# Kernel tuning notes

Measured on AMD Instinct MI355X. Metric: run time of the kernel, lower is better.

## Reference

```python
import jax, jax.numpy as jnp
import numpy as np

D_MODEL = 1024


def setup_inputs() -> dict:
    key = jax.random.key(0)
    kx, kq, kk, kv = jax.random.split(key, 4)
    x = jax.random.normal(kx, (4, 2048, D_MODEL), dtype=jnp.float32)
    s = 1.0 / np.sqrt(D_MODEL)
    # torch nn.Linear weight is [out, in]; y = x @ W.T
    Wq = jax.random.normal(kq, (D_MODEL, D_MODEL), dtype=jnp.float32) * s
    Wk = jax.random.normal(kk, (D_MODEL, D_MODEL), dtype=jnp.float32) * s
    Wv = jax.random.normal(kv, (D_MODEL, D_MODEL), dtype=jnp.float32) * s
    return {"x": x, "Wq": Wq, "Wk": Wk, "Wv": Wv}


def reference(x, Wq, Wk, Wv):
    # Linear projections (no bias): [b, s, d]
    Q = jnp.einsum("bsd,ed->bse", x, Wq)
    K = jnp.einsum("bsd,ed->bse", x, Wk)
    V = jnp.einsum("bsd,ed->bse", x, Wv)
    d_k = Q.shape[-1]
    scores = jnp.einsum("bqd,bkd->bqk", Q, K) / jnp.sqrt(jnp.asarray(d_k, Q.dtype))
    weights = jax.nn.softmax(scores, axis=-1)
    return jnp.einsum("bqk,bkd->bqd", weights, V)
```

## Files before the change

kernel.cpp:

```cpp
#include <hip/hip_runtime.h>
#include <hip/hip_bf16.h>

using bf16 = __hip_bfloat16;
typedef __attribute__((ext_vector_type(8))) short short8;
typedef __attribute__((ext_vector_type(16))) float f32x16;

__global__ __launch_bounds__(256) void cast_f32_to_bf16(const float* __restrict__ in,
                                                        bf16* __restrict__ out) {
  const int i = (blockIdx.x * 256 + threadIdx.x) * 4;
  const float4 f = *(const float4*)(in + i);
  bf16 h[4];
  h[0] = __float2bfloat16(f.x);
  h[1] = __float2bfloat16(f.y);
  h[2] = __float2bfloat16(f.z);
  h[3] = __float2bfloat16(f.w);
  *(uint2*)(out + i) = *(const uint2*)h;
}

__global__ __launch_bounds__(256) void cast_weights(const float* __restrict__ Wq,
                                                    const float* __restrict__ Wk,
                                                    const float* __restrict__ Wv,
                                                    bf16* __restrict__ out) {
  const int b = blockIdx.x;
  const float* src = (b < 1024) ? (Wq + (size_t)b * 1024)
                   : (b < 2048) ? (Wk + (size_t)(b - 1024) * 1024)
                                : (Wv + (size_t)(b - 2048) * 1024);
  const int i = threadIdx.x * 4;
  const float4 f = *(const float4*)(src + i);
  bf16 h[4];
  h[0] = __float2bfloat16(f.x);
  h[1] = __float2bfloat16(f.y);
  h[2] = __float2bfloat16(f.z);
  h[3] = __float2bfloat16(f.w);
  *(uint2*)(out + (size_t)b * 1024 + i) = *(const uint2*)h;
}

template <class Epi>
__device__ __forceinline__ void gemm128_nt(const bf16* __restrict__ A, const bf16* __restrict__ B,
                                           int lda, int ldb, int K, Epi epi) {
  __shared__ char smem[36864];
  bf16* As = (bf16*)smem;
  bf16* Bs = (bf16*)(smem + 8192);
  const int t = threadIdx.x;
  const int lane = t & 63;
  const int wave = t >> 6;
  const int wm = (wave >> 1) * 64;
  const int wn = (wave & 1) * 64;
  const int m0 = blockIdx.y * 128;
  const int n0 = blockIdx.x * 128;

  f32x16 acc[2][2];
#pragma unroll
  for (int i = 0; i < 2; ++i)
#pragma unroll
    for (int j = 0; j < 2; ++j)
#pragma unroll
      for (int r = 0; r < 16; ++r) acc[i][j][r] = 0.f;

  const int r0 = t >> 2;
  const int fsw = (r0 + (r0 >> 2)) & 3;
  const int cglob = ((t & 3) ^ fsw) << 3;
  const bf16* gA0 = A + (size_t)(m0 + r0) * lda + cglob;
  const bf16* gB0 = B + (size_t)(n0 + r0) * ldb + cglob;
  const bf16* gA1 = gA0 + (size_t)64 * lda;
  const bf16* gB1 = gB0 + (size_t)64 * ldb;
  bf16* lA = As + (size_t)wave * 64 * 8;
  bf16* lB = Bs + (size_t)wave * 64 * 8;

  const int rl = lane & 31;
  const int grp = lane >> 5;
  const int ffr = (rl + (rl >> 2)) & 3;

  for (int k0 = 0; k0 < K; k0 += 32) {
    __builtin_amdgcn_global_load_lds((const __attribute__((address_space(1))) unsigned int*)(gA0 + k0),
                                     (__attribute__((address_space(3))) unsigned int*)lA, 16, 0, 0);
    __builtin_amdgcn_global_load_lds((const __attribute__((address_space(1))) unsigned int*)(gB0 + k0),
                                     (__attribute__((address_space(3))) unsigned int*)lB, 16, 0, 0);
    __builtin_amdgcn_global_load_lds((const __attribute__((address_space(1))) unsigned int*)(gA1 + k0),
                                     (__attribute__((address_space(3))) unsigned int*)(lA + 2048), 16, 0, 0);
    __builtin_amdgcn_global_load_lds((const __attribute__((address_space(1))) unsigned int*)(gB1 + k0),
                                     (__attribute__((address_space(3))) unsigned int*)(lB + 2048), 16, 0, 0);
    __syncthreads();

    short8 af[2][2], bfr[2][2];
#pragma unroll
    for (int ks = 0; ks < 2; ++ks) {
      const int kb = ks * 2 + grp;
      const int co = ((kb ^ ffr) << 3);
#pragma unroll
      for (int mt = 0; mt < 2; ++mt)
        af[ks][mt] = *(const short8*)(As + (wm + mt * 32 + rl) * 32 + co);
#pragma unroll
      for (int nt = 0; nt < 2; ++nt)
        bfr[ks][nt] = *(const short8*)(Bs + (wn + nt * 32 + rl) * 32 + co);
    }
#pragma unroll
    for (int ks = 0; ks < 2; ++ks)
#pragma unroll
      for (int mt = 0; mt < 2; ++mt)
#pragma unroll
        for (int nt = 0; nt < 2; ++nt)
          acc[mt][nt] = __builtin_amdgcn_mfma_f32_32x32x16_bf16(af[ks][mt], bfr[ks][nt],
                                                                acc[mt][nt], 0, 0, 0);
    __syncthreads();
  }

  epi(acc, m0, n0, wm, wn, lane, wave, smem);
}

__device__ __forceinline__ int c_row(int reg, int lane) {
  return (reg & 3) + 8 * (reg >> 2) + 4 * (lane >> 5);
}

template <class F>
__device__ __forceinline__ void for_each_c(const f32x16 (&acc)[2][2], int m0, int n0, int wm,
                                           int wn, int lane, F f) {
  const int rl = lane & 31;
#pragma unroll
  for (int mt = 0; mt < 2; ++mt)
#pragma unroll
    for (int nt = 0; nt < 2; ++nt)
#pragma unroll
      for (int reg = 0; reg < 16; ++reg)
        f(m0 + wm + mt * 32 + c_row(reg, lane), n0 + wn + nt * 32 + rl, acc[mt][nt][reg]);
}

__global__ __launch_bounds__(256) void proj_kernel(const bf16* __restrict__ xb,
                                                   const bf16* __restrict__ Wb,
                                                   bf16* __restrict__ Qb, bf16* __restrict__ Kb,
                                                   bf16* __restrict__ Vt) {
  gemm128_nt(xb, Wb, 1024, 1024, 1024,
             [=](const f32x16 (&acc)[2][2], int m0, int n0, int wm, int wn, int lane, int wave,
                 char* smem) {
    if (n0 < 2048) {
      bf16* dst = (n0 < 1024) ? Qb : Kb;
      const int nb = (n0 < 1024) ? n0 : (n0 - 1024);
      for_each_c(acc, m0, nb, wm, wn, lane, [&](int m, int n, float v) {
        dst[(size_t)m * 1024 + n] = __float2bfloat16(v);
      });
    } else {
      bf16* T = (bf16*)smem + wave * 4608;
      const int rl = lane & 31;
      const int g4 = 4 * (lane >> 5);
#pragma unroll
      for (int mt = 0; mt < 2; ++mt)
#pragma unroll
        for (int nt = 0; nt < 2; ++nt)
#pragma unroll
          for (int q = 0; q < 4; ++q) {
            bf16 h4[4];
#pragma unroll
            for (int r = 0; r < 4; ++r) h4[r] = __float2bfloat16(acc[mt][nt][4 * q + r]);
            *(uint2*)(T + (nt * 32 + rl) * 72 + mt * 32 + 8 * q + g4) = *(const uint2*)h4;
          }
      asm volatile("s_waitcnt lgkmcnt(0)" ::: "memory");
      const int mbase = m0 + wm;
      const int bb = mbase >> 11;
      const int sbase = mbase & 2047;
      const int nvbase = n0 - 2048 + wn;
#pragma unroll
      for (int i = 0; i < 8; ++i) {
        const int nl = i * 8 + (lane >> 3);
        const int ml = (lane & 7) * 8;
        const short8 val = *(const short8*)(T + nl * 72 + ml);
        *(short8*)(Vt + ((size_t)bb * 1024 + nvbase + nl) * 2048 + sbase + ml) = val;
      }
    }
  });
}

__global__ __launch_bounds__(256) void qk_exp_kernel(const bf16* __restrict__ Qb,
                                                     const bf16* __restrict__ Kb,
                                                     bf16* __restrict__ E,
                                                     float* __restrict__ Lpart) {
  const int z = blockIdx.z;
  const bf16* A = Qb + (size_t)z * 2048 * 1024;
  const bf16* B = Kb + (size_t)z * 2048 * 1024;
  bf16* Ez = E + (size_t)z * 2048 * 2048;
  float* Lz = Lpart + (size_t)z * 16 * 2048;
  gemm128_nt(A, B, 1024, 1024, 1024,
             [=](const f32x16 (&acc)[2][2], int m0, int n0, int wm, int wn, int lane, int wave,
                 char* smem) {
    float* Lp = (float*)smem;
    const int rl = lane & 31;
#pragma unroll
    for (int mt = 0; mt < 2; ++mt)
#pragma unroll
      for (int reg = 0; reg < 16; ++reg) {
        const int mr = wm + mt * 32 + c_row(reg, lane);
        float s = 0.f;
#pragma unroll
        for (int nt = 0; nt < 2; ++nt) {
          const float e = __expf(acc[mt][nt][reg] * 0.03125f);
          Ez[(size_t)(m0 + mr) * 2048 + n0 + wn + nt * 32 + rl] = __float2bfloat16(e);
          s += e;
        }
        s += __shfl_xor(s, 1, 64);
        s += __shfl_xor(s, 2, 64);
        s += __shfl_xor(s, 4, 64);
        s += __shfl_xor(s, 8, 64);
        s += __shfl_xor(s, 16, 64);
        if (rl == 0) Lp[mr * 2 + (wave & 1)] = s;
      }
    __syncthreads();
    const int t = threadIdx.x;
    if (t < 128) Lz[(n0 >> 7) * 2048 + m0 + t] = Lp[t * 2 + 0] + Lp[t * 2 + 1];
  });
}

__global__ __launch_bounds__(256) void reduce_l_kernel(const float* __restrict__ Lpart,
                                                       float* __restrict__ invL) {
  const int i = blockIdx.x * 256 + threadIdx.x;
  const int z = i >> 11, m = i & 2047;
  const float* p = Lpart + (size_t)z * 16 * 2048 + m;
  float s = 0.f;
#pragma unroll
  for (int t = 0; t < 16; ++t) s += p[(size_t)t * 2048];
  invL[i] = 1.f / s;
}

__global__ __launch_bounds__(256) void pv_kernel(const bf16* __restrict__ E,
                                                 const bf16* __restrict__ Vt,
                                                 const float* __restrict__ invL,
                                                 float* __restrict__ out) {
  const int z = blockIdx.z;
  const bf16* A = E + (size_t)z * 2048 * 2048;
  const bf16* B = Vt + (size_t)z * 1024 * 2048;
  const float* ilz = invL + (size_t)z * 2048;
  float* oz = out + (size_t)z * 2048 * 1024;
  gemm128_nt(A, B, 2048, 2048, 2048,
             [=](const f32x16 (&acc)[2][2], int m0, int n0, int wm, int wn, int lane, int wave,
                 char* smem) {
    const int rl = lane & 31;
#pragma unroll
    for (int mt = 0; mt < 2; ++mt)
#pragma unroll
      for (int reg = 0; reg < 16; ++reg) {
        const int m = m0 + wm + mt * 32 + c_row(reg, lane);
        const float il = ilz[m];
#pragma unroll
        for (int nt = 0; nt < 2; ++nt)
          oz[(size_t)m * 1024 + n0 + wn + nt * 32 + rl] = acc[mt][nt][reg] * il;
      }
  });
}

extern "C" void kernel_launch(void* const* d_in, const int* in_sizes, int n_in,
                              void* d_out, int out_size, void* d_ws, size_t ws_size,
                              hipStream_t stream) {
  const float* x = (const float*)d_in[0];
  const float* Wq = (const float*)d_in[1];
  const float* Wk = (const float*)d_in[2];
  const float* Wv = (const float*)d_in[3];
  float* out = (float*)d_out;

  char* w = (char*)d_ws;
  bf16* xb = (bf16*)w; w += (size_t)8192 * 1024 * 2;
  bf16* Wb = (bf16*)w; w += (size_t)3072 * 1024 * 2;
  bf16* Qb = (bf16*)w; w += (size_t)8192 * 1024 * 2;
  bf16* Kb = (bf16*)w; w += (size_t)8192 * 1024 * 2;
  bf16* Vt = (bf16*)w; w += (size_t)8192 * 1024 * 2;
  bf16* E  = (bf16*)w; w += (size_t)4 * 2048 * 2048 * 2;
  float* Lpart = (float*)w; w += (size_t)4 * 16 * 2048 * 4;
  float* invL  = (float*)w; w += (size_t)4 * 2048 * 4;

  cast_f32_to_bf16<<<8192, 256, 0, stream>>>(x, xb);
  cast_weights<<<3072, 256, 0, stream>>>(Wq, Wk, Wv, Wb);

  proj_kernel<<<dim3(24, 64), 256, 0, stream>>>(xb, Wb, Qb, Kb, Vt);

  qk_exp_kernel<<<dim3(16, 16, 4), 256, 0, stream>>>(Qb, Kb, E, Lpart);
  reduce_l_kernel<<<32, 256, 0, stream>>>(Lpart, invL);

  pv_kernel<<<dim3(8, 16, 4), 256, 0, stream>>>(E, Vt, invL, out);
}
```

Baseline: 265.4 us.

## Double GEMM K-tile to 64, merge cast kernels, fold row-sum reduction into PV

The shared GEMM mainloop now stages a 64-wide K slice per iteration instead of 32. It uses a new 8-way XOR swizzle for global-to-LDS loads and fragment reads, which halves the number of barrier pairs per K. The two f32-to-bf16 cast kernels are merged into one launch. The separate softmax-denominator reduction kernel is removed: each PV block sums the 16 partials for its 128 rows into shared memory in its epilogue. This cuts launch overhead and synchronisation, at the cost of redundant partial-sum reads across the N blocks and a larger LDS footprint per stage.

```diff
diff --git a/kernel.cpp b/kernel.cpp
--- a/kernel.cpp
+++ b/kernel.cpp
@@ -5,26 +5,27 @@
 typedef __attribute__((ext_vector_type(8))) short short8;
 typedef __attribute__((ext_vector_type(16))) float f32x16;
 
-__global__ __launch_bounds__(256) void cast_f32_to_bf16(const float* __restrict__ in,
-                                                        bf16* __restrict__ out) {
-  const int i = (blockIdx.x * 256 + threadIdx.x) * 4;
-  const float4 f = *(const float4*)(in + i);
-  bf16 h[4];
-  h[0] = __float2bfloat16(f.x);
-  h[1] = __float2bfloat16(f.y);
-  h[2] = __float2bfloat16(f.z);
-  h[3] = __float2bfloat16(f.w);
-  *(uint2*)(out + i) = *(const uint2*)h;
-}
-
-__global__ __launch_bounds__(256) void cast_weights(const float* __restrict__ Wq,
-                                                    const float* __restrict__ Wk,
-                                                    const float* __restrict__ Wv,
-                                                    bf16* __restrict__ out) {
+__global__ __launch_bounds__(256) void cast_all(const float* __restrict__ x,
+                                                const float* __restrict__ Wq,
+                                                const float* __restrict__ Wk,
+                                                const float* __restrict__ Wv,
+                                                bf16* __restrict__ xb, bf16* __restrict__ Wb) {
   const int b = blockIdx.x;
-  const float* src = (b < 1024) ? (Wq + (size_t)b * 1024)
-                   : (b < 2048) ? (Wk + (size_t)(b - 1024) * 1024)
-                                : (Wv + (size_t)(b - 2048) * 1024);
+  const float* src;
+  bf16* dst;
+  if (b < 8192) {
+    src = x + (size_t)b * 1024;
+    dst = xb + (size_t)b * 1024;
+  } else if (b < 9216) {
+    src = Wq + (size_t)(b - 8192) * 1024;
+    dst = Wb + (size_t)(b - 8192) * 1024;
+  } else if (b < 10240) {
+    src = Wk + (size_t)(b - 9216) * 1024;
+    dst = Wb + (size_t)(b - 8192) * 1024;
+  } else {
+    src = Wv + (size_t)(b - 10240) * 1024;
+    dst = Wb + (size_t)(b - 8192) * 1024;
+  }
   const int i = threadIdx.x * 4;
   const float4 f = *(const float4*)(src + i);
   bf16 h[4];
@@ -32,7 +33,7 @@
   h[1] = __float2bfloat16(f.y);
   h[2] = __float2bfloat16(f.z);
   h[3] = __float2bfloat16(f.w);
-  *(uint2*)(out + (size_t)b * 1024 + i) = *(const uint2*)h;
+  *(uint2*)(dst + i) = *(const uint2*)h;
 }
 
 template <class Epi>
@@ -40,7 +41,7 @@
                                            int lda, int ldb, int K, Epi epi) {
   __shared__ char smem[36864];
   bf16* As = (bf16*)smem;
-  bf16* Bs = (bf16*)(smem + 8192);
+  bf16* Bs = (bf16*)(smem + 16384);
   const int t = threadIdx.x;
   const int lane = t & 63;
   const int wave = t >> 6;
@@ -57,50 +58,51 @@
 #pragma unroll
       for (int r = 0; r < 16; ++r) acc[i][j][r] = 0.f;
 
-  const int r0 = t >> 2;
-  const int fsw = (r0 + (r0 >> 2)) & 3;
-  const int cglob = ((t & 3) ^ fsw) << 3;
-  const bf16* gA0 = A + (size_t)(m0 + r0) * lda + cglob;
-  const bf16* gB0 = B + (size_t)(n0 + r0) * ldb + cglob;
-  const bf16* gA1 = gA0 + (size_t)64 * lda;
-  const bf16* gB1 = gB0 + (size_t)64 * ldb;
-  bf16* lA = As + (size_t)wave * 64 * 8;
-  bf16* lB = Bs + (size_t)wave * 64 * 8;
+  const bf16* gA[4];
+  const bf16* gB[4];
+#pragma unroll
+  for (int j = 0; j < 4; ++j) {
+    const int row = j * 32 + wave * 8 + (lane >> 3);
+    const int f = ((lane >> 3) + j * 4 + wave) & 7;
+    const int c = (((lane & 7) ^ f)) << 3;
+    gA[j] = A + (size_t)(m0 + row) * lda + c;
+    gB[j] = B + (size_t)(n0 + row) * ldb + c;
+  }
 
   const int rl = lane & 31;
   const int grp = lane >> 5;
-  const int ffr = (rl + (rl >> 2)) & 3;
-
-  for (int k0 = 0; k0 < K; k0 += 32) {
-    __builtin_amdgcn_global_load_lds((const __attribute__((address_space(1))) unsigned int*)(gA0 + k0),
-                                     (__attribute__((address_space(3))) unsigned int*)lA, 16, 0, 0);
-    __builtin_amdgcn_global_load_lds((const __attribute__((address_space(1))) unsigned int*)(gB0 + k0),
-                                     (__attribute__((address_space(3))) unsigned int*)lB, 16, 0, 0);
-    __builtin_amdgcn_global_load_lds((const __attribute__((address_space(1))) unsigned int*)(gA1 + k0),
-                                     (__attribute__((address_space(3))) unsigned int*)(lA + 2048), 16, 0, 0);
-    __builtin_amdgcn_global_load_lds((const __attribute__((address_space(1))) unsigned int*)(gB1 + k0),
-                                     (__attribute__((address_space(3))) unsigned int*)(lB + 2048), 16, 0, 0);
-    __syncthreads();
-
-    short8 af[2][2], bfr[2][2];
-#pragma unroll
-    for (int ks = 0; ks < 2; ++ks) {
+
+  for (int k0 = 0; k0 < K; k0 += 64) {
+#pragma unroll
+    for (int j = 0; j < 4; ++j) {
+      __builtin_amdgcn_global_load_lds(
+          (const __attribute__((address_space(1))) unsigned int*)(gA[j] + k0),
+          (__attribute__((address_space(3))) unsigned int*)(As + (j * 4 + wave) * 512), 16, 0, 0);
+      __builtin_amdgcn_global_load_lds(
+          (const __attribute__((address_space(1))) unsigned int*)(gB[j] + k0),
+          (__attribute__((address_space(3))) unsigned int*)(Bs + (j * 4 + wave) * 512), 16, 0, 0);
+    }
+    __syncthreads();
+
+    short8 af[4][2], bv[4][2];
+#pragma unroll
+    for (int ks = 0; ks < 4; ++ks) {
       const int kb = ks * 2 + grp;
-      const int co = ((kb ^ ffr) << 3);
+#pragma unroll
+      for (int mt = 0; mt < 2; ++mt) {
+        const int fm = (rl + (rl >> 3) + mt * 4) & 7;
+        const int co = (kb ^ fm) << 3;
+        af[ks][mt] = *(const short8*)(As + (wm + mt * 32 + rl) * 64 + co);
+        bv[ks][mt] = *(const short8*)(Bs + (wn + mt * 32 + rl) * 64 + co);
+      }
+    }
+#pragma unroll
+    for (int ks = 0; ks < 4; ++ks)
 #pragma unroll
       for (int mt = 0; mt < 2; ++mt)
-        af[ks][mt] = *(const short8*)(As + (wm + mt * 32 + rl) * 32 + co);
-#pragma unroll
-      for (int nt = 0; nt < 2; ++nt)
-        bfr[ks][nt] = *(const short8*)(Bs + (wn + nt * 32 + rl) * 32 + co);
-    }
-#pragma unroll
-    for (int ks = 0; ks < 2; ++ks)
-#pragma unroll
-      for (int mt = 0; mt < 2; ++mt)
 #pragma unroll
         for (int nt = 0; nt < 2; ++nt)
-          acc[mt][nt] = __builtin_amdgcn_mfma_f32_32x32x16_bf16(af[ks][mt], bfr[ks][nt],
+          acc[mt][nt] = __builtin_amdgcn_mfma_f32_32x32x16_bf16(af[ks][mt], bv[ks][nt],
                                                                 acc[mt][nt], 0, 0, 0);
     __syncthreads();
   }
@@ -208,39 +210,37 @@
   });
 }
 
-__global__ __launch_bounds__(256) void reduce_l_kernel(const float* __restrict__ Lpart,
-                                                       float* __restrict__ invL) {
-  const int i = blockIdx.x * 256 + threadIdx.x;
-  const int z = i >> 11, m = i & 2047;
-  const float* p = Lpart + (size_t)z * 16 * 2048 + m;
-  float s = 0.f;
-#pragma unroll
-  for (int t = 0; t < 16; ++t) s += p[(size_t)t * 2048];
-  invL[i] = 1.f / s;
-}
-
 __global__ __launch_bounds__(256) void pv_kernel(const bf16* __restrict__ E,
                                                  const bf16* __restrict__ Vt,
-                                                 const float* __restrict__ invL,
+                                                 const float* __restrict__ Lpart,
                                                  float* __restrict__ out) {
   const int z = blockIdx.z;
   const bf16* A = E + (size_t)z * 2048 * 2048;
   const bf16* B = Vt + (size_t)z * 1024 * 2048;
-  const float* ilz = invL + (size_t)z * 2048;
+  const float* Lz = Lpart + (size_t)z * 16 * 2048;
   float* oz = out + (size_t)z * 2048 * 1024;
   gemm128_nt(A, B, 2048, 2048, 2048,
              [=](const f32x16 (&acc)[2][2], int m0, int n0, int wm, int wn, int lane, int wave,
                  char* smem) {
+    float* Lsm = (float*)smem;
+    const int t = threadIdx.x;
+    if (t < 128) {
+      float s = 0.f;
+#pragma unroll
+      for (int i = 0; i < 16; ++i) s += Lz[(size_t)i * 2048 + m0 + t];
+      Lsm[t] = 1.f / s;
+    }
+    __syncthreads();
     const int rl = lane & 31;
 #pragma unroll
     for (int mt = 0; mt < 2; ++mt)
 #pragma unroll
       for (int reg = 0; reg < 16; ++reg) {
-        const int m = m0 + wm + mt * 32 + c_row(reg, lane);
-        const float il = ilz[m];
+        const int ml = wm + mt * 32 + c_row(reg, lane);
+        const float il = Lsm[ml];
 #pragma unroll
         for (int nt = 0; nt < 2; ++nt)
-          oz[(size_t)m * 1024 + n0 + wn + nt * 32 + rl] = acc[mt][nt][reg] * il;
+          oz[(size_t)(m0 + ml) * 1024 + n0 + wn + nt * 32 + rl] = acc[mt][nt][reg] * il;
       }
   });
 }
@@ -262,15 +262,12 @@
   bf16* Vt = (bf16*)w; w += (size_t)8192 * 1024 * 2;
   bf16* E  = (bf16*)w; w += (size_t)4 * 2048 * 2048 * 2;
   float* Lpart = (float*)w; w += (size_t)4 * 16 * 2048 * 4;
-  float* invL  = (float*)w; w += (size_t)4 * 2048 * 4;
-
-  cast_f32_to_bf16<<<8192, 256, 0, stream>>>(x, xb);
-  cast_weights<<<3072, 256, 0, stream>>>(Wq, Wk, Wv, Wb);
+
+  cast_all<<<11264, 256, 0, stream>>>(x, Wq, Wk, Wv, xb, Wb);
 
   proj_kernel<<<dim3(24, 64), 256, 0, stream>>>(xb, Wb, Qb, Kb, Vt);
 
   qk_exp_kernel<<<dim3(16, 16, 4), 256, 0, stream>>>(Qb, Kb, E, Lpart);
-  reduce_l_kernel<<<32, 256, 0, stream>>>(Lpart, invL);
-
-  pv_kernel<<<dim3(8, 16, 4), 256, 0, stream>>>(E, Vt, invL, out);
-}
+
+  pv_kernel<<<dim3(8, 16, 4), 256, 0, stream>>>(E, Vt, Lpart, out);
+}
```

New measurement: 251.4 us. -5.3%, faster.
